# Optimization experiments

Hardware: AMD Instinct MI355X
Metric: run time of the kernel (lower is better)

The kernel has to match this reference:

```python
import jax, jax.numpy as jnp
import numpy as np

B, N, P, D = 32, 8, 6, 96
E, H, I, K, NL = 128, 8, 64, 32, 2
L = N * D  # transformer sequence length = 768
OUT = 128
EPS = 1e-5


def _layernorm(x, s, b):
    m = jnp.mean(x, axis=-1, keepdims=True)
    v = jnp.mean((x - m) ** 2, axis=-1, keepdims=True)
    return (x - m) / jnp.sqrt(v + EPS) * s + b


def _pos_encoding(length, d_model):
    pos = jnp.arange(length, dtype=jnp.float32)[:, None]
    div = jnp.exp(jnp.arange(0, d_model, 2, dtype=jnp.float32) * (-jnp.log(10000.0) / d_model))
    ang = pos * div  # [L, E/2]
    return jnp.stack([jnp.sin(ang), jnp.cos(ang)], axis=-1).reshape(length, d_model)


def setup_inputs() -> dict:
    key = jax.random.key(0)
    ks = jax.random.split(key, 20)
    s = 0.02
    return {
        "x": jax.random.normal(ks[0], (B, N, P, D), jnp.float32),
        "prototypes": jax.random.normal(ks[1], (D, K, P), jnp.float32),
        "emb_w": jax.random.normal(ks[2], (E, P), jnp.float32) * s,
        "emb_b": jnp.zeros((E,), jnp.float32),
        "proj_w": jax.random.normal(ks[3], (E, P), jnp.float32) * s,
        "proj_b": jnp.zeros((E,), jnp.float32),
        "in_proj_w": jax.random.normal(ks[4], (NL, 3 * E, E), jnp.float32) * s,
        "in_proj_b": jnp.zeros((NL, 3 * E), jnp.float32),
        "out_proj_w": jax.random.normal(ks[5], (NL, E, E), jnp.float32) * s,
        "out_proj_b": jnp.zeros((NL, E), jnp.float32),
        "ln1_s": jnp.ones((NL, E), jnp.float32),
        "ln1_b": jnp.zeros((NL, E), jnp.float32),
        "ffn_w1": jax.random.normal(ks[6], (NL, I, E), jnp.float32) * s,
        "ffn_b1": jnp.zeros((NL, I), jnp.float32),
        "ffn_w2": jax.random.normal(ks[7], (NL, E, I), jnp.float32) * s,
        "ffn_b2": jnp.zeros((NL, E), jnp.float32),
        "ln2_s": jnp.ones((NL, E), jnp.float32),
        "ln2_b": jnp.zeros((NL, E), jnp.float32),
        "out_w": jax.random.normal(ks[8], (OUT, L * E), jnp.float32) * s,
        "out_b": jnp.zeros((OUT,), jnp.float32),
    }


def reference(x, prototypes, emb_w, emb_b, proj_w, proj_b,
              in_proj_w, in_proj_b, out_proj_w, out_proj_b,
              ln1_s, ln1_b, ffn_w1, ffn_b1, ffn_w2, ffn_b2,
              ln2_s, ln2_b, out_w, out_b):
    # Faithful to torch .view: raw row-major reinterpretation [B,N,P,D] -> [B*N*D, P]
    x_flat = x.reshape(B * N * D, P)
    x_normed = x_flat / jnp.maximum(jnp.linalg.norm(x_flat, axis=1, keepdims=True), 1e-12)
    x_norm = x_normed.reshape(B, N, D, P)
    p_normed = prototypes / jnp.maximum(jnp.linalg.norm(prototypes, axis=2, keepdims=True), 1e-12)

    # Vectorized per-dim cosine-sim argmax + gather (replaces the Python loop over D)
    sim = jnp.einsum('bndp,dkp->bndk', x_norm, p_normed)  # [B,N,D,K]
    best_idx = jnp.argmax(sim, axis=3)                    # [B,N,D]
    d_idx = jnp.arange(D)[None, None, :]
    selected = p_normed[d_idx, best_idx]                  # [B,N,D,P]

    input_embed = (x_flat @ emb_w.T + emb_b).reshape(B, N, D, E)
    proto_embed = (selected.reshape(B * N * D, P) @ proj_w.T + proj_b).reshape(B, N, D, E)
    seq = (input_embed + proto_embed).reshape(B, L, E)
    seq = seq + _pos_encoding(L, E)[None]

    scale = 1.0 / jnp.sqrt(jnp.float32(E // H))
    for l in range(NL):
        qkv = seq @ in_proj_w[l].T + in_proj_b[l]          # [B,L,3E]
        q, k, v = jnp.split(qkv, 3, axis=-1)
        q = q.reshape(B, L, H, E // H)
        k = k.reshape(B, L, H, E // H)
        v = v.reshape(B, L, H, E // H)
        logits = jnp.einsum('blhd,bmhd->bhlm', q, k) * scale
        attn = jax.nn.softmax(logits, axis=-1)
        ctx = jnp.einsum('bhlm,bmhd->blhd', attn, v).reshape(B, L, E)
        attn_out = ctx @ out_proj_w[l].T + out_proj_b[l]
        seq = _layernorm(seq + attn_out, ln1_s[l], ln1_b[l])
        h = jax.nn.elu(seq @ ffn_w1[l].T + ffn_b1[l])
        ffn_out = h @ ffn_w2[l].T + ffn_b2[l]
        seq = _layernorm(seq + ffn_out, ln2_s[l], ln2_b[l])

    z = seq.reshape(B, L * E)
    return z @ out_w.T + out_b
```

## Files before the change

### kernel.cpp

```cpp
#include <hip/hip_runtime.h>
#include <hip/hip_bf16.h>
#include <math.h>

typedef unsigned short ushort_t;
typedef unsigned int uint_t;

#define BB 32
#define PP 6
#define DD 96
#define EE 128
#define HH 8
#define II 64
#define KK 32
#define LSEQ 768
#define ROWS (BB * LSEQ)
#define OUTN 128
#define KOUT (LSEQ * EE)

using bf16x8 = __attribute__((ext_vector_type(8))) short;
using bf16x4 = __attribute__((ext_vector_type(4))) short;
using f32x4  = __attribute__((ext_vector_type(4))) float;
using u32x4  = __attribute__((ext_vector_type(4))) uint_t;

__device__ __forceinline__ ushort_t f2b(float f) {
    __hip_bfloat16 h = __float2bfloat16(f);
    return *reinterpret_cast<ushort_t*>(&h);
}
__device__ __forceinline__ uint_t permpack(float hi, float lo) {
    return __builtin_amdgcn_perm(__builtin_bit_cast(uint_t, hi),
                                 __builtin_bit_cast(uint_t, lo), 0x07060302u);
}

__global__ void cast_all_kernel(
    const float* __restrict__ s0, int n0, const float* __restrict__ s1, int n1,
    const float* __restrict__ s2, int n2, const float* __restrict__ s3, int n3,
    ushort_t* __restrict__ d0, ushort_t* __restrict__ d1,
    ushort_t* __restrict__ d2, ushort_t* __restrict__ d3,
    float* __restrict__ peT)
{
    int i = blockIdx.x * 256 + threadIdx.x;
    if (i < n0) { d0[i] = f2b(s0[i]); return; }
    i -= n0;
    if (i < n1) { d1[i] = f2b(s1[i]); return; }
    i -= n1;
    if (i < n2) { d2[i] = f2b(s2[i]); return; }
    i -= n2;
    if (i < n3) { d3[i] = f2b(s3[i]); return; }
    i -= n3;
    const int lpos = i >> 7, tt = i & 127;
    const float twoj = (float)((tt >> 1) * 2);
    const float div = __expf(twoj * (-9.210340371976184f / 128.0f));
    const float ang = (float)lpos * div;
    peT[i] = (tt & 1) ? __cosf(ang) : __sinf(ang);
}

__global__ __launch_bounds__(128) void embed_kernel(
    const float* __restrict__ x, const float* __restrict__ prot,
    const float* __restrict__ emb_w, const float* __restrict__ emb_b,
    const float* __restrict__ proj_w, const float* __restrict__ proj_b,
    const float* __restrict__ peT,
    float* __restrict__ seq, ushort_t* __restrict__ seq_bf)
{
    const int r = blockIdx.x;
    const int t = threadIdx.x;
    __shared__ float xrow[PP];
    __shared__ float sel[PP];

    if (t < PP) xrow[t] = x[r * PP + t];
    __syncthreads();

    float nx = 0.f;
    #pragma unroll
    for (int p = 0; p < PP; ++p) nx += xrow[p] * xrow[p];
    const float xinv = 1.f / fmaxf(sqrtf(nx), 1e-12f);

    const int d = r % DD;
    if (t < KK) {
        const float* pr = prot + (d * KK + t) * PP;
        float pp[PP];
        float np2 = 0.f;
        #pragma unroll
        for (int p = 0; p < PP; ++p) { pp[p] = pr[p]; np2 += pp[p] * pp[p]; }
        const float pinv = 1.f / fmaxf(sqrtf(np2), 1e-12f);
        float dot = 0.f;
        #pragma unroll
        for (int p = 0; p < PP; ++p) dot += xrow[p] * pp[p];
        float sim = dot * xinv * pinv;
        int k = t;
        #pragma unroll
        for (int off = 16; off; off >>= 1) {
            float osim = __shfl_down(sim, off);
            int   ok   = __shfl_down(k, off);
            if (osim > sim || (osim == sim && ok < k)) { sim = osim; k = ok; }
        }
        k = __shfl(k, 0);
        if (t == k) {
            #pragma unroll
            for (int p = 0; p < PP; ++p) sel[p] = pp[p] * pinv;
        }
    }
    __syncthreads();

    float acc = emb_b[t] + proj_b[t];
    #pragma unroll
    for (int p = 0; p < PP; ++p) acc = fmaf(xrow[p], emb_w[t * PP + p], acc);
    #pragma unroll
    for (int p = 0; p < PP; ++p) acc = fmaf(sel[p], proj_w[t * PP + p], acc);

    const int lpos = r % LSEQ;
    const float v = acc + peT[lpos * EE + t];
    seq[(size_t)r * EE + t] = v;
    seq_bf[(size_t)r * EE + t] = f2b(v);
}

__global__ __launch_bounds__(256) void gemm_qkv(
    const ushort_t* __restrict__ A, const ushort_t* __restrict__ W,
    const float* __restrict__ bias,
    ushort_t* __restrict__ q_bf, ushort_t* __restrict__ k2,
    ushort_t* __restrict__ v2)
{
    __shared__ ushort_t Ws[64 * 136];
    const int t = threadIdx.x;
    const int wave = t >> 6, lane = t & 63;
    const int quad = lane >> 4, l16 = lane & 15;
    const int m0 = blockIdx.y * 128, n0 = blockIdx.x * 64;

    for (int c = t; c < 64 * 16; c += 256) {
        int row = c >> 4, col = c & 15;
        *(bf16x8*)&Ws[row * 136 + col * 8] =
            *(const bf16x8*)&W[(size_t)(n0 + row) * 128 + col * 8];
    }
    __syncthreads();

    f32x4 acc[2][4];
    #pragma unroll
    for (int s = 0; s < 2; ++s)
        #pragma unroll
        for (int nt = 0; nt < 4; ++nt)
            acc[s][nt] = (f32x4){0.f, 0.f, 0.f, 0.f};

    const ushort_t* a0p = A + (size_t)(m0 + wave * 32 + l16) * 128 + quad * 8;
    const ushort_t* a1p = a0p + (size_t)16 * 128;
    const ushort_t* wp  = &Ws[l16 * 136 + quad * 8];

    #pragma unroll
    for (int k0 = 0; k0 < 128; k0 += 32) {
        bf16x8 a0 = *(const bf16x8*)(a0p + k0);
        bf16x8 a1 = *(const bf16x8*)(a1p + k0);
        #pragma unroll
        for (int nt = 0; nt < 4; ++nt) {
            bf16x8 wf = *(const bf16x8*)(wp + nt * 16 * 136 + k0);
            acc[0][nt] = __builtin_amdgcn_mfma_f32_16x16x32_bf16(wf, a0, acc[0][nt], 0, 0, 0);
            acc[1][nt] = __builtin_amdgcn_mfma_f32_16x16x32_bf16(wf, a1, acc[1][nt], 0, 0, 0);
        }
    }

    const int b = blockIdx.y / 6;
    #pragma unroll
    for (int s = 0; s < 2; ++s) {
        const int m = m0 + wave * 32 + s * 16 + l16;
        const int l = m - b * LSEQ;
        const int c4 = l >> 4, r16 = l & 15;
        #pragma unroll
        for (int nt = 0; nt < 4; ++nt) {
            const int nb = n0 + nt * 16 + quad * 4;
            float4 b4 = *(const float4*)&bias[nb];
            float v[4];
            #pragma unroll
            for (int r = 0; r < 4; ++r)
                v[r] = acc[s][nt][r] + ((const float*)&b4)[r];

            if (n0 < 128) {
                #pragma unroll
                for (int r = 0; r < 4; ++r) v[r] *= 0.36067376022224085f;
                uint2 w2;
                w2.x = permpack(v[1], v[0]);
                w2.y = permpack(v[3], v[2]);
                *(uint2*)&q_bf[(size_t)m * EE + nb] = w2;
            } else if (n0 < 256) {
                const int h = ((n0 - 128) >> 4) + nt;
                uint2 w2;
                w2.x = permpack(v[1], v[0]);
                w2.y = permpack(v[3], v[2]);
                *(uint2*)&k2[((((size_t)(b * HH + h)) * 48 + c4) * 4 + quad) * 64 + r16 * 4] = w2;
            } else {
                const int h = ((n0 - 256) >> 4) + nt;
                const size_t vbase = (((size_t)(b * HH + h)) * 48 + c4) * 16;
                #pragma unroll
                for (int r = 0; r < 4; ++r)
                    v2[(vbase + quad * 4 + r) * 16 + r16] = f2b(v[r]);
            }
        }
    }
}

__device__ __forceinline__ void attn_step(
    bf16x4 kf, bf16x4 vf, const bf16x4 (&qf)[2],
    f32x4 (&oacc)[2], f32x4 (&lacc)[2], bf16x4 ones4)
{
    const f32x4 zero4 = (f32x4){0.f, 0.f, 0.f, 0.f};
    #pragma unroll
    for (int s = 0; s < 2; ++s) {
        f32x4 sv = __builtin_amdgcn_mfma_f32_16x16x16bf16_1k(kf, qf[s], zero4, 0, 0, 0);
        float e0 = __builtin_amdgcn_exp2f(sv[0]);
        float e1 = __builtin_amdgcn_exp2f(sv[1]);
        float e2 = __builtin_amdgcn_exp2f(sv[2]);
        float e3 = __builtin_amdgcn_exp2f(sv[3]);
        uint2 pu;
        pu.x = permpack(e1, e0);
        pu.y = permpack(e3, e2);
        bf16x4 pf = __builtin_bit_cast(bf16x4, pu);
        oacc[s] = __builtin_amdgcn_mfma_f32_16x16x16bf16_1k(vf, pf, oacc[s], 0, 0, 0);
        lacc[s] = __builtin_amdgcn_mfma_f32_16x16x16bf16_1k(ones4, pf, lacc[s], 0, 0, 0);
    }
}

__global__ __launch_bounds__(256) void attention_mfma(
    const ushort_t* __restrict__ q_bf, const ushort_t* __restrict__ k2,
    const ushort_t* __restrict__ v2, ushort_t* __restrict__ ctx)
{
    const int bh = blockIdx.x;
    const int b = bh & 31, h = bh >> 5;
    const int qb = blockIdx.y;
    const int t = threadIdx.x;
    const int wave = t >> 6, lane = t & 63;
    const int quad = lane >> 4, l16 = lane & 15;
    const int hoff = h * 16;

    bf16x4 qf[2];
    #pragma unroll
    for (int s = 0; s < 2; ++s) {
        int row = b * LSEQ + qb * 128 + wave * 32 + s * 16 + l16;
        qf[s] = *(const bf16x4*)&q_bf[(size_t)row * EE + hoff + quad * 4];
    }

    const int bhn = b * HH + h;
    const ushort_t* kp = k2 + (size_t)bhn * 12288 + quad * 64 + l16 * 4;
    const ushort_t* vp = v2 + (size_t)bhn * 12288 + l16 * 16 + quad * 4;

    f32x4 oacc[2], lacc[2];
    oacc[0] = (f32x4){0.f, 0.f, 0.f, 0.f};
    oacc[1] = (f32x4){0.f, 0.f, 0.f, 0.f};
    lacc[0] = (f32x4){0.f, 0.f, 0.f, 0.f};
    lacc[1] = (f32x4){0.f, 0.f, 0.f, 0.f};
    bf16x4 ones4;
    #pragma unroll
    for (int j = 0; j < 4; ++j) ones4[j] = (short)0x3F80;

    bf16x4 kb0 = *(const bf16x4*)(kp);
    bf16x4 vb0 = *(const bf16x4*)(vp);
    bf16x4 kb1 = *(const bf16x4*)(kp + 256);
    bf16x4 vb1 = *(const bf16x4*)(vp + 256);
    bf16x4 kb2 = *(const bf16x4*)(kp + 512);
    bf16x4 vb2 = *(const bf16x4*)(vp + 512);
    bf16x4 kb3 = *(const bf16x4*)(kp + 768);
    bf16x4 vb3 = *(const bf16x4*)(vp + 768);

    for (int c0 = 0; c0 < 48; c0 += 4) {
        attn_step(kb0, vb0, qf, oacc, lacc, ones4);
        { int n = c0 + 4; n = n >= 48 ? n - 48 : n;
          kb0 = *(const bf16x4*)(kp + n * 256); vb0 = *(const bf16x4*)(vp + n * 256); }
        attn_step(kb1, vb1, qf, oacc, lacc, ones4);
        { int n = c0 + 5; n = n >= 48 ? n - 48 : n;
          kb1 = *(const bf16x4*)(kp + n * 256); vb1 = *(const bf16x4*)(vp + n * 256); }
        attn_step(kb2, vb2, qf, oacc, lacc, ones4);
        { int n = c0 + 6; n = n >= 48 ? n - 48 : n;
          kb2 = *(const bf16x4*)(kp + n * 256); vb2 = *(const bf16x4*)(vp + n * 256); }
        attn_step(kb3, vb3, qf, oacc, lacc, ones4);
        { int n = c0 + 7; n = n >= 48 ? n - 48 : n;
          kb3 = *(const bf16x4*)(kp + n * 256); vb3 = *(const bf16x4*)(vp + n * 256); }
    }

    #pragma unroll
    for (int s = 0; s < 2; ++s) {
        const float inv = 1.f / lacc[s][0];
        const int q = qb * 128 + wave * 32 + s * 16 + l16;
        uint2 w2;
        w2.x = permpack(oacc[s][1] * inv, oacc[s][0] * inv);
        w2.y = permpack(oacc[s][3] * inv, oacc[s][2] * inv);
        *(uint2*)&ctx[((size_t)(b * LSEQ + q)) * EE + hoff + quad * 4] = w2;
    }
}

#define W1OFF 0
#define W2OFF 8704
#define YOFF  17920
#define HOFF  26624
__global__ __launch_bounds__(256) void gemm_ln_ffn(
    const ushort_t* __restrict__ ctx_bf, const ushort_t* __restrict__ Wout,
    const float* __restrict__ bout,
    const float* __restrict__ g1, const float* __restrict__ be1,
    const ushort_t* __restrict__ W1, const float* __restrict__ b1,
    const ushort_t* __restrict__ W2, const float* __restrict__ b2,
    const float* __restrict__ g2, const float* __restrict__ be2,
    float* __restrict__ seq, ushort_t* __restrict__ seq_bf, int write_f32)
{
    __shared__ ushort_t S[31232];
    const int t = threadIdx.x;
    const int wave = t >> 6, lane = t & 63;
    const int quad = lane >> 4, l16 = lane & 15;
    const int m0 = blockIdx.x * 64;
    const int lrow = wave * 16 + l16;
    const int m = m0 + lrow;

    for (int c = t; c < 128 * 16; c += 256) {
        int row = c >> 4, col = c & 15;
        *(bf16x8*)&S[row * 136 + col * 8] =
            *(const bf16x8*)&Wout[(size_t)row * 128 + col * 8];
    }
    __syncthreads();

    f32x4 acc[8];
    #pragma unroll
    for (int nt = 0; nt < 8; ++nt) acc[nt] = (f32x4){0.f, 0.f, 0.f, 0.f};
    {
        const ushort_t* ap = ctx_bf + (size_t)m * EE + quad * 8;
        const ushort_t* wp = &S[l16 * 136 + quad * 8];
        #pragma unroll
        for (int k0 = 0; k0 < 128; k0 += 32) {
            bf16x8 a = *(const bf16x8*)(ap + k0);
            #pragma unroll
            for (int nt = 0; nt < 8; ++nt) {
                bf16x8 wf = *(const bf16x8*)(wp + nt * 16 * 136 + k0);
                acc[nt] = __builtin_amdgcn_mfma_f32_16x16x32_bf16(wf, a, acc[nt], 0, 0, 0);
            }
        }
    }
    __syncthreads();

    for (int c = t; c < 64 * 16; c += 256) {
        int row = c >> 4, col = c & 15;
        *(bf16x8*)&S[W1OFF + row * 136 + col * 8] =
            *(const bf16x8*)&W1[(size_t)row * 128 + col * 8];
    }
    for (int c = t; c < 128 * 8; c += 256) {
        int row = c >> 3, col = c & 7;
        *(bf16x8*)&S[W2OFF + row * 72 + col * 8] =
            *(const bf16x8*)&W2[(size_t)row * 64 + col * 8];
    }

    float y[8][4];
    float s = 0.f;
    #pragma unroll
    for (int nt = 0; nt < 8; ++nt) {
        const int nb = nt * 16 + quad * 4;
        float4 b4 = *(const float4*)&bout[nb];
        float4 r4 = *(const float4*)&seq[(size_t)m * EE + nb];
        #pragma unroll
        for (int r = 0; r < 4; ++r) {
            y[nt][r] = acc[nt][r] + ((const float*)&b4)[r] + ((const float*)&r4)[r];
            s += y[nt][r];
        }
    }
    s += __shfl_xor(s, 16);
    s += __shfl_xor(s, 32);
    float mean = s * (1.f / 128.f);
    float s2 = 0.f;
    #pragma unroll
    for (int nt = 0; nt < 8; ++nt)
        #pragma unroll
        for (int r = 0; r < 4; ++r) {
            float d = y[nt][r] - mean;
            s2 += d * d;
        }
    s2 += __shfl_xor(s2, 16);
    s2 += __shfl_xor(s2, 32);
    float rstd = 1.f / sqrtf(s2 * (1.f / 128.f) + 1e-5f);

    #pragma unroll
    for (int nt = 0; nt < 8; ++nt) {
        const int nb = nt * 16 + quad * 4;
        float4 g4 = *(const float4*)&g1[nb];
        float4 be4 = *(const float4*)&be1[nb];
        #pragma unroll
        for (int r = 0; r < 4; ++r)
            y[nt][r] = (y[nt][r] - mean) * rstd * ((const float*)&g4)[r] + ((const float*)&be4)[r];
        uint2 w2;
        w2.x = permpack(y[nt][1], y[nt][0]);
        w2.y = permpack(y[nt][3], y[nt][2]);
        *(uint2*)&S[YOFF + lrow * 136 + nb] = w2;
    }
    __syncthreads();

    f32x4 acc1[4];
    #pragma unroll
    for (int nt = 0; nt < 4; ++nt) acc1[nt] = (f32x4){0.f, 0.f, 0.f, 0.f};
    {
        const ushort_t* ap1 = &S[YOFF + lrow * 136 + quad * 8];
        const ushort_t* w1p = &S[W1OFF + l16 * 136 + quad * 8];
        #pragma unroll
        for (int k0 = 0; k0 < 128; k0 += 32) {
            bf16x8 a = *(const bf16x8*)(ap1 + k0);
            #pragma unroll
            for (int nt = 0; nt < 4; ++nt) {
                bf16x8 wf = *(const bf16x8*)(w1p + nt * 16 * 136 + k0);
                acc1[nt] = __builtin_amdgcn_mfma_f32_16x16x32_bf16(wf, a, acc1[nt], 0, 0, 0);
            }
        }
    }
    #pragma unroll
    for (int nt = 0; nt < 4; ++nt) {
        const int ib = nt * 16 + quad * 4;
        float4 b4 = *(const float4*)&b1[ib];
        float hv[4];
        #pragma unroll
        for (int r = 0; r < 4; ++r) {
            float u = acc1[nt][r] + ((const float*)&b4)[r];
            hv[r] = u > 0.f ? u : expm1f(u);
        }
        uint2 w2;
        w2.x = permpack(hv[1], hv[0]);
        w2.y = permpack(hv[3], hv[2]);
        *(uint2*)&S[HOFF + lrow * 72 + ib] = w2;
    }

    f32x4 acc2[8];
    #pragma unroll
    for (int nt = 0; nt < 8; ++nt) acc2[nt] = (f32x4){0.f, 0.f, 0.f, 0.f};
    {
        const ushort_t* hp  = &S[HOFF + lrow * 72 + quad * 8];
        const ushort_t* w2p = &S[W2OFF + l16 * 72 + quad * 8];
        #pragma unroll
        for (int k0 = 0; k0 < 64; k0 += 32) {
            bf16x8 hf = *(const bf16x8*)(hp + k0);
            #pragma unroll
            for (int nt = 0; nt < 8; ++nt) {
                bf16x8 wf = *(const bf16x8*)(w2p + nt * 16 * 72 + k0);
                acc2[nt] = __builtin_amdgcn_mfma_f32_16x16x32_bf16(wf, hf, acc2[nt], 0, 0, 0);
            }
        }
    }

    float v[8][4];
    s = 0.f;
    #pragma unroll
    for (int nt = 0; nt < 8; ++nt) {
        const int nb = nt * 16 + quad * 4;
        float4 b4 = *(const float4*)&b2[nb];
        #pragma unroll
        for (int r = 0; r < 4; ++r) {
            v[nt][r] = acc2[nt][r] + ((const float*)&b4)[r] + y[nt][r];
            s += v[nt][r];
        }
    }
    s += __shfl_xor(s, 16);
    s += __shfl_xor(s, 32);
    mean = s * (1.f / 128.f);
    s2 = 0.f;
    #pragma unroll
    for (int nt = 0; nt < 8; ++nt)
        #pragma unroll
        for (int r = 0; r < 4; ++r) {
            float d = v[nt][r] - mean;
            s2 += d * d;
        }
    s2 += __shfl_xor(s2, 16);
    s2 += __shfl_xor(s2, 32);
    rstd = 1.f / sqrtf(s2 * (1.f / 128.f) + 1e-5f);

    #pragma unroll
    for (int nt = 0; nt < 8; ++nt) {
        const int nb = nt * 16 + quad * 4;
        float4 g4 = *(const float4*)&g2[nb];
        float4 be4 = *(const float4*)&be2[nb];
        float o[4];
        #pragma unroll
        for (int r = 0; r < 4; ++r)
            o[r] = (v[nt][r] - mean) * rstd * ((const float*)&g4)[r] + ((const float*)&be4)[r];
        if (write_f32) {
            float4 f4 = {o[0], o[1], o[2], o[3]};
            *(float4*)&seq[(size_t)m * EE + nb] = f4;
        }
        uint2 w2;
        w2.x = permpack(o[1], o[0]);
        w2.y = permpack(o[3], o[2]);
        *(uint2*)&seq_bf[(size_t)m * EE + nb] = w2;
    }
}

#define PKC 384
#define PNBLK (KOUT / PKC)
__global__ __launch_bounds__(256) void out_gemm3(
    const ushort_t* __restrict__ seqbf, const float* __restrict__ out_w,
    float* __restrict__ part)
{
    const int t = threadIdx.x;
    const int wave = t >> 6, lane = t & 63;
    const int quad = lane >> 4, l16 = lane & 15;
    const size_t k0 = (size_t)blockIdx.x * PKC;
    const int n0 = wave * 32;

    f32x4 acc[2][2];
    #pragma unroll
    for (int mt = 0; mt < 2; ++mt)
        #pragma unroll
        for (int nt = 0; nt < 2; ++nt)
            acc[mt][nt] = (f32x4){0.f, 0.f, 0.f, 0.f};

    const ushort_t* a0p = seqbf + (size_t)l16 * KOUT + k0 + quad * 8;
    const ushort_t* a1p = a0p + (size_t)16 * KOUT;
    const float* w0p = out_w + (size_t)(n0 + l16) * KOUT + k0 + quad * 8;
    const float* w1p = w0p + (size_t)16 * KOUT;

    for (int ks = 0; ks < PKC; ks += 32) {
        bf16x8 a0 = *(const bf16x8*)(a0p + ks);
        bf16x8 a1 = *(const bf16x8*)(a1p + ks);
        float4 wa0 = *(const float4*)(w0p + ks);
        float4 wa1 = *(const float4*)(w0p + ks + 4);
        float4 wb0 = *(const float4*)(w1p + ks);
        float4 wb1 = *(const float4*)(w1p + ks + 4);
        u32x4 b0, b1;
        b0[0] = permpack(wa0.y, wa0.x); b0[1] = permpack(wa0.w, wa0.z);
        b0[2] = permpack(wa1.y, wa1.x); b0[3] = permpack(wa1.w, wa1.z);
        b1[0] = permpack(wb0.y, wb0.x); b1[1] = permpack(wb0.w, wb0.z);
        b1[2] = permpack(wb1.y, wb1.x); b1[3] = permpack(wb1.w, wb1.z);
        bf16x8 bf0 = __builtin_bit_cast(bf16x8, b0);
        bf16x8 bf1 = __builtin_bit_cast(bf16x8, b1);
        acc[0][0] = __builtin_amdgcn_mfma_f32_16x16x32_bf16(a0, bf0, acc[0][0], 0, 0, 0);
        acc[1][0] = __builtin_amdgcn_mfma_f32_16x16x32_bf16(a1, bf0, acc[1][0], 0, 0, 0);
        acc[0][1] = __builtin_amdgcn_mfma_f32_16x16x32_bf16(a0, bf1, acc[0][1], 0, 0, 0);
        acc[1][1] = __builtin_amdgcn_mfma_f32_16x16x32_bf16(a1, bf1, acc[1][1], 0, 0, 0);
    }

    float* pb = part + (size_t)blockIdx.x * (32 * 128);
    #pragma unroll
    for (int mt = 0; mt < 2; ++mt)
        #pragma unroll
        for (int nt = 0; nt < 2; ++nt)
            #pragma unroll
            for (int r = 0; r < 4; ++r)
                pb[(mt * 16 + quad * 4 + r) * 128 + n0 + nt * 16 + l16] = acc[mt][nt][r];
}

__global__ __launch_bounds__(256) void out_reduce(
    const float* __restrict__ part, const float* __restrict__ out_b,
    float* __restrict__ out)
{
    const int i = blockIdx.x * 256 + threadIdx.x;
    const float* p = part + i;
    float s0 = 0.f, s1 = 0.f, s2 = 0.f, s3 = 0.f;
    for (int blk = 0; blk < PNBLK; blk += 4) {
        s0 += p[(size_t)blk * 4096];
        s1 += p[(size_t)(blk + 1) * 4096];
        s2 += p[(size_t)(blk + 2) * 4096];
        s3 += p[(size_t)(blk + 3) * 4096];
    }
    out[i] = out_b[i & (OUTN - 1)] + ((s0 + s1) + (s2 + s3));
}

extern "C" void kernel_launch(void* const* d_in, const int* in_sizes, int n_in,
                              void* d_out, int out_size, void* d_ws, size_t ws_size,
                              hipStream_t stream)
{
    const float* x          = (const float*)d_in[0];
    const float* prototypes = (const float*)d_in[1];
    const float* emb_w      = (const float*)d_in[2];
    const float* emb_b      = (const float*)d_in[3];
    const float* proj_w     = (const float*)d_in[4];
    const float* proj_b     = (const float*)d_in[5];
    const float* in_proj_w  = (const float*)d_in[6];
    const float* in_proj_b  = (const float*)d_in[7];
    const float* out_proj_w = (const float*)d_in[8];
    const float* out_proj_b = (const float*)d_in[9];
    const float* ln1_s      = (const float*)d_in[10];
    const float* ln1_b      = (const float*)d_in[11];
    const float* ffn_w1     = (const float*)d_in[12];
    const float* ffn_b1     = (const float*)d_in[13];
    const float* ffn_w2     = (const float*)d_in[14];
    const float* ffn_b2     = (const float*)d_in[15];
    const float* ln2_s      = (const float*)d_in[16];
    const float* ln2_b      = (const float*)d_in[17];
    const float* out_w      = (const float*)d_in[18];
    const float* out_b      = (const float*)d_in[19];
    float* out = (float*)d_out;
    char* base = (char*)d_ws;

    float*    seq    = (float*)base;
    float*    tmp    = (float*)(base + 12582912);
    ushort_t* seq_bf = (ushort_t*)(base + 25165824);
    ushort_t* q_bf   = (ushort_t*)(base + 31457280);
    ushort_t* k2     = (ushort_t*)(base + 37748736);
    ushort_t* v2     = (ushort_t*)(base + 44040192);
    ushort_t* ctx_bf = (ushort_t*)(base + 50331648);
    ushort_t* w_bf   = (ushort_t*)(base + 56623104);
    float*    part   = tmp;
    float*    peT    = (float*)(base + 12582912 + 9437184);
    (void)ws_size;

    ushort_t* w_in  = w_bf;
    ushort_t* w_out = w_bf + 98304;
    ushort_t* w_f1  = w_bf + 131072;
    ushort_t* w_f2  = w_bf + 147456;

    cast_all_kernel<<<1024, 256, 0, stream>>>(
        in_proj_w, 98304, out_proj_w, 32768, ffn_w1, 16384, ffn_w2, 16384,
        w_in, w_out, w_f1, w_f2, peT);

    embed_kernel<<<ROWS, 128, 0, stream>>>(x, prototypes, emb_w, emb_b,
                                           proj_w, proj_b, peT, seq, seq_bf);

    for (int l = 0; l < 2; ++l) {
        gemm_qkv<<<dim3(6, 192), 256, 0, stream>>>(
            seq_bf, w_in + (size_t)l * 49152, in_proj_b + l * 384,
            q_bf, k2, v2);
        attention_mfma<<<dim3(BB * HH, 6), 256, 0, stream>>>(q_bf, k2, v2, ctx_bf);
        gemm_ln_ffn<<<ROWS / 64, 256, 0, stream>>>(
            ctx_bf, w_out + (size_t)l * 16384, out_proj_b + l * 128,
            ln1_s + l * EE, ln1_b + l * EE,
            w_f1 + (size_t)l * 8192, ffn_b1 + l * II,
            w_f2 + (size_t)l * 8192, ffn_b2 + l * EE,
            ln2_s + l * EE, ln2_b + l * EE,
            seq, seq_bf, l == 0 ? 1 : 0);
    }

    out_gemm3<<<PNBLK, 256, 0, stream>>>(seq_bf, out_w, part);
    out_reduce<<<BB * OUTN / 256, 256, 0, stream>>>(part, out_b, out);
}
```

Baseline: 282.4 us.

## Fuse cast with embed, use K=32 MFMA in attention, split output reduction

```diff
diff --git a/kernel.cpp b/kernel.cpp
--- a/kernel.cpp
+++ b/kernel.cpp
@@ -31,86 +31,81 @@
                                  __builtin_bit_cast(uint_t, lo), 0x07060302u);
 }
 
-__global__ void cast_all_kernel(
+#define NCAST 320
+__global__ __launch_bounds__(512) void cast_embed_kernel(
     const float* __restrict__ s0, int n0, const float* __restrict__ s1, int n1,
     const float* __restrict__ s2, int n2, const float* __restrict__ s3, int n3,
     ushort_t* __restrict__ d0, ushort_t* __restrict__ d1,
     ushort_t* __restrict__ d2, ushort_t* __restrict__ d3,
-    float* __restrict__ peT)
-{
-    int i = blockIdx.x * 256 + threadIdx.x;
-    if (i < n0) { d0[i] = f2b(s0[i]); return; }
-    i -= n0;
-    if (i < n1) { d1[i] = f2b(s1[i]); return; }
-    i -= n1;
-    if (i < n2) { d2[i] = f2b(s2[i]); return; }
-    i -= n2;
-    if (i < n3) { d3[i] = f2b(s3[i]); return; }
-    i -= n3;
-    const int lpos = i >> 7, tt = i & 127;
-    const float twoj = (float)((tt >> 1) * 2);
-    const float div = __expf(twoj * (-9.210340371976184f / 128.0f));
-    const float ang = (float)lpos * div;
-    peT[i] = (tt & 1) ? __cosf(ang) : __sinf(ang);
-}
-
-__global__ __launch_bounds__(128) void embed_kernel(
     const float* __restrict__ x, const float* __restrict__ prot,
     const float* __restrict__ emb_w, const float* __restrict__ emb_b,
     const float* __restrict__ proj_w, const float* __restrict__ proj_b,
-    const float* __restrict__ peT,
     float* __restrict__ seq, ushort_t* __restrict__ seq_bf)
 {
-    const int r = blockIdx.x;
-    const int t = threadIdx.x;
-    __shared__ float xrow[PP];
-    __shared__ float sel[PP];
-
-    if (t < PP) xrow[t] = x[r * PP + t];
-    __syncthreads();
-
+    if (blockIdx.x < NCAST) {
+        int i = blockIdx.x * 512 + threadIdx.x;
+        if (i < n0) { d0[i] = f2b(s0[i]); return; }
+        i -= n0;
+        if (i < n1) { d1[i] = f2b(s1[i]); return; }
+        i -= n1;
+        if (i < n2) { d2[i] = f2b(s2[i]); return; }
+        i -= n2;
+        if (i < n3) { d3[i] = f2b(s3[i]); }
+        return;
+    }
+
+    const int wave = threadIdx.x >> 6, lane = threadIdx.x & 63;
+    const int r = (blockIdx.x - NCAST) * 8 + wave;
+    const int d = r % DD;
+    const int lpos = r % LSEQ;
+
+    float xr[PP];
     float nx = 0.f;
     #pragma unroll
-    for (int p = 0; p < PP; ++p) nx += xrow[p] * xrow[p];
+    for (int p = 0; p < PP; ++p) { xr[p] = x[r * PP + p]; nx += xr[p] * xr[p]; }
     const float xinv = 1.f / fmaxf(sqrtf(nx), 1e-12f);
 
-    const int d = r % DD;
-    if (t < KK) {
-        const float* pr = prot + (d * KK + t) * PP;
-        float pp[PP];
-        float np2 = 0.f;
-        #pragma unroll
-        for (int p = 0; p < PP; ++p) { pp[p] = pr[p]; np2 += pp[p] * pp[p]; }
-        const float pinv = 1.f / fmaxf(sqrtf(np2), 1e-12f);
-        float dot = 0.f;
-        #pragma unroll
-        for (int p = 0; p < PP; ++p) dot += xrow[p] * pp[p];
-        float sim = dot * xinv * pinv;
-        int k = t;
-        #pragma unroll
-        for (int off = 16; off; off >>= 1) {
-            float osim = __shfl_down(sim, off);
-            int   ok   = __shfl_down(k, off);
-            if (osim > sim || (osim == sim && ok < k)) { sim = osim; k = ok; }
-        }
-        k = __shfl(k, 0);
-        if (t == k) {
-            #pragma unroll
-            for (int p = 0; p < PP; ++p) sel[p] = pp[p] * pinv;
-        }
-    }
-    __syncthreads();
-
-    float acc = emb_b[t] + proj_b[t];
-    #pragma unroll
-    for (int p = 0; p < PP; ++p) acc = fmaf(xrow[p], emb_w[t * PP + p], acc);
-    #pragma unroll
-    for (int p = 0; p < PP; ++p) acc = fmaf(sel[p], proj_w[t * PP + p], acc);
-
-    const int lpos = r % LSEQ;
-    const float v = acc + peT[lpos * EE + t];
-    seq[(size_t)r * EE + t] = v;
-    seq_bf[(size_t)r * EE + t] = f2b(v);
+    const int tk = lane & 31;
+    const float* pr = prot + (d * KK + tk) * PP;
+    float np2 = 0.f, dot = 0.f;
+    #pragma unroll
+    for (int p = 0; p < PP; ++p) {
+        float pv = pr[p];
+        np2 += pv * pv;
+        dot += xr[p] * pv;
+    }
+    const float pinv = 1.f / fmaxf(sqrtf(np2), 1e-12f);
+    float sim = dot * xinv * pinv;
+    int k = tk;
+    #pragma unroll
+    for (int off = 16; off; off >>= 1) {
+        float osim = __shfl_xor(sim, off);
+        int   ok   = __shfl_xor(k, off);
+        if (osim > sim || (osim == sim && ok < k)) { sim = osim; k = ok; }
+    }
+    const float* sr = prot + (d * KK + k) * PP;
+    float sp[PP], sn2 = 0.f;
+    #pragma unroll
+    for (int p = 0; p < PP; ++p) { sp[p] = sr[p]; sn2 += sp[p] * sp[p]; }
+    const float spinv = 1.f / fmaxf(sqrtf(sn2), 1e-12f);
+
+    #pragma unroll
+    for (int c = 0; c < 2; ++c) {
+        const int t = lane + c * 64;
+        float acc = emb_b[t] + proj_b[t];
+        #pragma unroll
+        for (int p = 0; p < PP; ++p) {
+            acc = fmaf(xr[p], emb_w[t * PP + p], acc);
+            acc = fmaf(sp[p] * spinv, proj_w[t * PP + p], acc);
+        }
+        const float twoj = (float)((t >> 1) * 2);
+        const float div = __expf(twoj * (-9.210340371976184f / 128.0f));
+        const float ang = (float)lpos * div;
+        const float pe = (t & 1) ? __cosf(ang) : __sinf(ang);
+        const float v = acc + pe;
+        seq[(size_t)r * EE + t] = v;
+        seq_bf[(size_t)r * EE + t] = f2b(v);
+    }
 }
 
 __global__ __launch_bounds__(256) void gemm_qkv(
@@ -160,7 +155,7 @@
     for (int s = 0; s < 2; ++s) {
         const int m = m0 + wave * 32 + s * 16 + l16;
         const int l = m - b * LSEQ;
-        const int c4 = l >> 4, r16 = l & 15;
+        const int c32 = l >> 5, u = l & 31;
         #pragma unroll
         for (int nt = 0; nt < 4; ++nt) {
             const int nb = n0 + nt * 16 + quad * 4;
@@ -179,39 +174,48 @@
                 *(uint2*)&q_bf[(size_t)m * EE + nb] = w2;
             } else if (n0 < 256) {
                 const int h = ((n0 - 128) >> 4) + nt;
+                const int half = (u >> 2) & 1;
+                const int mm = ((u >> 3) << 2) | (u & 3);
                 uint2 w2;
                 w2.x = permpack(v[1], v[0]);
                 w2.y = permpack(v[3], v[2]);
-                *(uint2*)&k2[((((size_t)(b * HH + h)) * 48 + c4) * 4 + quad) * 64 + r16 * 4] = w2;
+                *(uint2*)&k2[((((((size_t)(b * HH + h)) * 24 + c32) * 2 + half) * 4 + quad) * 16 + mm) * 4] = w2;
             } else {
                 const int h = ((n0 - 256) >> 4) + nt;
-                const size_t vbase = (((size_t)(b * HH + h)) * 48 + c4) * 16;
+                const size_t vb = (((size_t)(b * HH + h)) * 24 + c32) * 512;
                 #pragma unroll
                 for (int r = 0; r < 4; ++r)
-                    v2[(vbase + quad * 4 + r) * 16 + r16] = f2b(v[r]);
+                    v2[vb + (quad * 4 + r) * 32 + u] = f2b(v[r]);
             }
         }
     }
 }
 
-__device__ __forceinline__ void attn_step(
-    bf16x4 kf, bf16x4 vf, const bf16x4 (&qf)[2],
-    f32x4 (&oacc)[2], f32x4 (&lacc)[2], bf16x4 ones4)
+__device__ __forceinline__ void attn_step32(
+    bf16x4 kf0, bf16x4 kf1, bf16x8 vf, const bf16x4 (&qf)[2],
+    f32x4 (&oacc)[2], f32x4 (&lacc)[2], bf16x8 ones8)
 {
     const f32x4 zero4 = (f32x4){0.f, 0.f, 0.f, 0.f};
     #pragma unroll
     for (int s = 0; s < 2; ++s) {
-        f32x4 sv = __builtin_amdgcn_mfma_f32_16x16x16bf16_1k(kf, qf[s], zero4, 0, 0, 0);
-        float e0 = __builtin_amdgcn_exp2f(sv[0]);
-        float e1 = __builtin_amdgcn_exp2f(sv[1]);
-        float e2 = __builtin_amdgcn_exp2f(sv[2]);
-        float e3 = __builtin_amdgcn_exp2f(sv[3]);
-        uint2 pu;
-        pu.x = permpack(e1, e0);
-        pu.y = permpack(e3, e2);
-        bf16x4 pf = __builtin_bit_cast(bf16x4, pu);
-        oacc[s] = __builtin_amdgcn_mfma_f32_16x16x16bf16_1k(vf, pf, oacc[s], 0, 0, 0);
-        lacc[s] = __builtin_amdgcn_mfma_f32_16x16x16bf16_1k(ones4, pf, lacc[s], 0, 0, 0);
+        f32x4 sv0 = __builtin_amdgcn_mfma_f32_16x16x16bf16_1k(kf0, qf[s], zero4, 0, 0, 0);
+        f32x4 sv1 = __builtin_amdgcn_mfma_f32_16x16x16bf16_1k(kf1, qf[s], zero4, 0, 0, 0);
+        float e0 = __builtin_amdgcn_exp2f(sv0[0]);
+        float e1 = __builtin_amdgcn_exp2f(sv0[1]);
+        float e2 = __builtin_amdgcn_exp2f(sv0[2]);
+        float e3 = __builtin_amdgcn_exp2f(sv0[3]);
+        float e4 = __builtin_amdgcn_exp2f(sv1[0]);
+        float e5 = __builtin_amdgcn_exp2f(sv1[1]);
+        float e6 = __builtin_amdgcn_exp2f(sv1[2]);
+        float e7 = __builtin_amdgcn_exp2f(sv1[3]);
+        u32x4 pu;
+        pu[0] = permpack(e1, e0);
+        pu[1] = permpack(e3, e2);
+        pu[2] = permpack(e5, e4);
+        pu[3] = permpack(e7, e6);
+        bf16x8 pf = __builtin_bit_cast(bf16x8, pu);
+        oacc[s] = __builtin_amdgcn_mfma_f32_16x16x32_bf16(vf, pf, oacc[s], 0, 0, 0);
+        lacc[s] = __builtin_amdgcn_mfma_f32_16x16x32_bf16(ones8, pf, lacc[s], 0, 0, 0);
     }
 }
 
@@ -236,39 +240,43 @@
 
     const int bhn = b * HH + h;
     const ushort_t* kp = k2 + (size_t)bhn * 12288 + quad * 64 + l16 * 4;
-    const ushort_t* vp = v2 + (size_t)bhn * 12288 + l16 * 16 + quad * 4;
+    const ushort_t* vp = v2 + (size_t)bhn * 12288 + l16 * 32 + quad * 8;
 
     f32x4 oacc[2], lacc[2];
     oacc[0] = (f32x4){0.f, 0.f, 0.f, 0.f};
     oacc[1] = (f32x4){0.f, 0.f, 0.f, 0.f};
     lacc[0] = (f32x4){0.f, 0.f, 0.f, 0.f};
     lacc[1] = (f32x4){0.f, 0.f, 0.f, 0.f};
-    bf16x4 ones4;
-    #pragma unroll
-    for (int j = 0; j < 4; ++j) ones4[j] = (short)0x3F80;
-
-    bf16x4 kb0 = *(const bf16x4*)(kp);
-    bf16x4 vb0 = *(const bf16x4*)(vp);
-    bf16x4 kb1 = *(const bf16x4*)(kp + 256);
-    bf16x4 vb1 = *(const bf16x4*)(vp + 256);
-    bf16x4 kb2 = *(const bf16x4*)(kp + 512);
-    bf16x4 vb2 = *(const bf16x4*)(vp + 512);
-    bf16x4 kb3 = *(const bf16x4*)(kp + 768);
-    bf16x4 vb3 = *(const bf16x4*)(vp + 768);
-
-    for (int c0 = 0; c0 < 48; c0 += 4) {
-        attn_step(kb0, vb0, qf, oacc, lacc, ones4);
-        { int n = c0 + 4; n = n >= 48 ? n - 48 : n;
-          kb0 = *(const bf16x4*)(kp + n * 256); vb0 = *(const bf16x4*)(vp + n * 256); }
-        attn_step(kb1, vb1, qf, oacc, lacc, ones4);
-        { int n = c0 + 5; n = n >= 48 ? n - 48 : n;
-          kb1 = *(const bf16x4*)(kp + n * 256); vb1 = *(const bf16x4*)(vp + n * 256); }
-        attn_step(kb2, vb2, qf, oacc, lacc, ones4);
-        { int n = c0 + 6; n = n >= 48 ? n - 48 : n;
-          kb2 = *(const bf16x4*)(kp + n * 256); vb2 = *(const bf16x4*)(vp + n * 256); }
-        attn_step(kb3, vb3, qf, oacc, lacc, ones4);
-        { int n = c0 + 7; n = n >= 48 ? n - 48 : n;
-          kb3 = *(const bf16x4*)(kp + n * 256); vb3 = *(const bf16x4*)(vp + n * 256); }
+    bf16x8 ones8;
+    #pragma unroll
+    for (int j = 0; j < 8; ++j) ones8[j] = (short)0x3F80;
+
+    bf16x4 k0a = *(const bf16x4*)(kp);
+    bf16x4 k1a = *(const bf16x4*)(kp + 256);
+    bf16x8 va  = *(const bf16x8*)(vp);
+    bf16x4 k0b = *(const bf16x4*)(kp + 512);
+    bf16x4 k1b = *(const bf16x4*)(kp + 768);
+    bf16x8 vb  = *(const bf16x8*)(vp + 512);
+    bf16x4 k0c = *(const bf16x4*)(kp + 1024);
+    bf16x4 k1c = *(const bf16x4*)(kp + 1280);
+    bf16x8 vc  = *(const bf16x8*)(vp + 1024);
+
+    for (int c0 = 0; c0 < 24; c0 += 3) {
+        attn_step32(k0a, k1a, va, qf, oacc, lacc, ones8);
+        { int n = c0 + 3; if (n >= 24) n -= 24;
+          k0a = *(const bf16x4*)(kp + n * 512);
+          k1a = *(const bf16x4*)(kp + n * 512 + 256);
+          va  = *(const bf16x8*)(vp + n * 512); }
+        attn_step32(k0b, k1b, vb, qf, oacc, lacc, ones8);
+        { int n = c0 + 4; if (n >= 24) n -= 24;
+          k0b = *(const bf16x4*)(kp + n * 512);
+          k1b = *(const bf16x4*)(kp + n * 512 + 256);
+          vb  = *(const bf16x8*)(vp + n * 512); }
+        attn_step32(k0c, k1c, vc, qf, oacc, lacc, ones8);
+        { int n = c0 + 5; if (n >= 24) n -= 24;
+          k0c = *(const bf16x4*)(kp + n * 512);
+          k1c = *(const bf16x4*)(kp + n * 512 + 256);
+          vc  = *(const bf16x8*)(vp + n * 512); }
     }
 
     #pragma unroll
@@ -532,20 +540,31 @@
                 pb[(mt * 16 + quad * 4 + r) * 128 + n0 + nt * 16 + l16] = acc[mt][nt][r];
 }
 
-__global__ __launch_bounds__(256) void out_reduce(
-    const float* __restrict__ part, const float* __restrict__ out_b,
-    float* __restrict__ out)
-{
-    const int i = blockIdx.x * 256 + threadIdx.x;
-    const float* p = part + i;
+__global__ __launch_bounds__(256) void out_reduce1(
+    const float* __restrict__ part, float* __restrict__ part2)
+{
+    const int g = blockIdx.x & 15, sp = blockIdx.x >> 4;
+    const int i = g * 256 + threadIdx.x;
+    const float* p = part + (size_t)sp * 32 * 4096 + i;
     float s0 = 0.f, s1 = 0.f, s2 = 0.f, s3 = 0.f;
-    for (int blk = 0; blk < PNBLK; blk += 4) {
+    for (int blk = 0; blk < 32; blk += 4) {
         s0 += p[(size_t)blk * 4096];
         s1 += p[(size_t)(blk + 1) * 4096];
         s2 += p[(size_t)(blk + 2) * 4096];
         s3 += p[(size_t)(blk + 3) * 4096];
     }
-    out[i] = out_b[i & (OUTN - 1)] + ((s0 + s1) + (s2 + s3));
+    part2[sp * 4096 + i] = (s0 + s1) + (s2 + s3);
+}
+
+__global__ __launch_bounds__(256) void out_reduce2(
+    const float* __restrict__ part2, const float* __restrict__ out_b,
+    float* __restrict__ out)
+{
+    const int i = blockIdx.x * 256 + threadIdx.x;
+    float s = 0.f;
+    #pragma unroll
+    for (int sp = 0; sp < 8; ++sp) s += part2[sp * 4096 + i];
+    out[i] = out_b[i & (OUTN - 1)] + s;
 }
 
 extern "C" void kernel_launch(void* const* d_in, const int* in_sizes, int n_in,
@@ -584,7 +603,7 @@
     ushort_t* ctx_bf = (ushort_t*)(base + 50331648);
     ushort_t* w_bf   = (ushort_t*)(base + 56623104);
     float*    part   = tmp;
-    float*    peT    = (float*)(base + 12582912 + 9437184);
+    float*    part2  = (float*)(base + 12582912 + 8388608);
     (void)ws_size;
 
     ushort_t* w_in  = w_bf;
@@ -592,12 +611,10 @@
     ushort_t* w_f1  = w_bf + 131072;
     ushort_t* w_f2  = w_bf + 147456;
 
-    cast_all_kernel<<<1024, 256, 0, stream>>>(
+    cast_embed_kernel<<<NCAST + ROWS / 8, 512, 0, stream>>>(
         in_proj_w, 98304, out_proj_w, 32768, ffn_w1, 16384, ffn_w2, 16384,
-        w_in, w_out, w_f1, w_f2, peT);
-
-    embed_kernel<<<ROWS, 128, 0, stream>>>(x, prototypes, emb_w, emb_b,
-                                           proj_w, proj_b, peT, seq, seq_bf);
+        w_in, w_out, w_f1, w_f2,
+        x, prototypes, emb_w, emb_b, proj_w, proj_b, seq, seq_bf);
 
     for (int l = 0; l < 2; ++l) {
         gemm_qkv<<<dim3(6, 192), 256, 0, stream>>>(
@@ -614,5 +631,6 @@
     }
 
     out_gemm3<<<PNBLK, 256, 0, stream>>>(seq_bf, out_w, part);
-    out_reduce<<<BB * OUTN / 256, 256, 0, stream>>>(part, out_b, out);
-}
+    out_reduce1<<<128, 256, 0, stream>>>(part, part2);
+    out_reduce2<<<BB * OUTN / 256, 256, 0, stream>>>(part2, out_b, out);
+}
```

Result: faster. 260.9 us (-7.6%).
